# Kernel tuning notes

Hardware: AMD Instinct MI355X
Metric: run time of the kernel (lower is better)

The kernel has to match this reference:

```python
import math
import jax, jax.numpy as jnp
import numpy as np

S, B, H = 512, 64, 1024

def setup_inputs() -> dict:
    key = jax.random.key(0)
    ks = jax.random.split(key, 7)
    hidden = jax.random.normal(ks[0], (1, B, H), dtype=jnp.float32)
    encoder_outputs = jax.random.normal(ks[1], (S, B, H), dtype=jnp.float32)
    pe = jax.random.normal(ks[2], (B, S), dtype=jnp.float32)
    seq_mask = jax.random.bernoulli(ks[3], 0.1, (B, S))
    # nn.Linear(2H, H): weight (H, 2H), bias (H); nn.Linear(H, 1, bias=False): weight (1, H)
    Wa = jax.random.normal(ks[4], (H, 2 * H), dtype=jnp.float32) * (1.0 / math.sqrt(2 * H))
    ba = jax.random.normal(ks[5], (H,), dtype=jnp.float32) * 0.01
    Ws = jax.random.normal(ks[6], (1, H), dtype=jnp.float32) * (1.0 / math.sqrt(H))
    return {"hidden": hidden, "encoder_outputs": encoder_outputs, "pe": pe,
            "seq_mask": seq_mask, "Wa": Wa, "ba": ba, "Ws": Ws}

def reference(hidden, encoder_outputs, pe, seq_mask, Wa, ba, Ws):
    max_len, bsz, hdim = encoder_outputs.shape
    factor = 1.0 / math.sqrt(hdim)
    scale = factor * math.log(max_len)
    # repeat hidden along seq dim, concat on feature dim -> (S, B, 2H)
    h_rep = jnp.broadcast_to(hidden, (max_len, bsz, hdim))
    energy_in = jnp.concatenate([h_rep, encoder_outputs], axis=2)  # (S, B, 2H)
    e = jax.nn.relu(jnp.einsum('sbf,hf->sbh', energy_in, Wa) + ba)  # (S, B, H)
    attn = scale * jnp.einsum('sbh,oh->sbo', e, Ws)[..., 0]          # (S, B)
    attn = attn.T + pe                                               # (B, S)
    attn = jnp.where(seq_mask, jnp.float32(-1e12), attn)
    attn = jax.nn.softmax(attn, axis=1)
    return attn[:, None, :]  # (B, 1, S)
```

## Files before the change

### kernel.cpp

```cpp
#include <hip/hip_runtime.h>
#include <hip/hip_bf16.h>

#define S_LEN 512
#define HDIM 1024
#define H2 2048

typedef float f32x4 __attribute__((ext_vector_type(4)));
typedef float f32x2 __attribute__((ext_vector_type(2)));
typedef __bf16 bf16x8 __attribute__((ext_vector_type(8)));

#define E1_PITCH 258
__global__ __launch_bounds__(256) void k_e1(const float* __restrict__ hidden,
                                            const float* __restrict__ Wa,
                                            const float* __restrict__ ba,
                                            float* __restrict__ e1) {
    __shared__ float hsh[64 * E1_PITCH];
    int h = blockIdx.x * 4 + (threadIdx.x >> 6);
    int lane = threadIdx.x & 63;
    const float* wrow = Wa + (size_t)h * H2;
    float acc = 0.f;
    for (int k0 = 0; k0 < HDIM; k0 += 256) {
        __syncthreads();
        for (int idx = threadIdx.x; idx < 4096; idx += 256) {
            int b = idx >> 6, ck = (idx & 63) << 2;
            f32x4 v = *(const f32x4*)(hidden + b * HDIM + k0 + ck);
            f32x2 lo; lo[0] = v[0]; lo[1] = v[1];
            f32x2 hi; hi[0] = v[2]; hi[1] = v[3];
            *(f32x2*)(hsh + b * E1_PITCH + ck) = lo;
            *(f32x2*)(hsh + b * E1_PITCH + ck + 2) = hi;
        }
        __syncthreads();
        const float* wr = wrow + k0;
        const float* hb = hsh + lane * E1_PITCH;
#pragma unroll 8
        for (int kk = 0; kk < 256; kk += 4) {
            f32x4 w = *(const f32x4*)(wr + kk);
            f32x2 h01 = *(const f32x2*)(hb + kk);
            f32x2 h23 = *(const f32x2*)(hb + kk + 2);
            acc += w[0] * h01[0] + w[1] * h01[1] + w[2] * h23[0] + w[3] * h23[1];
        }
    }
    e1[lane * HDIM + h] = acc + ba[h];
}

__global__ __launch_bounds__(256) void k_packB(const float* __restrict__ Wa,
                                               unsigned short* __restrict__ wsB,
                                               float* __restrict__ logits) {
    int ci = blockIdx.x * 256 + threadIdx.x;
    if (ci < S_LEN * 64) logits[ci] = 0.f;
    int tile = ci >> 9;
    int wi = ci & 511;
    int row = wi >> 2;
    int slot = wi & 3;
    int nt = tile >> 5, kt = tile & 31;
    int n = nt * 128 + row;
    int kk = kt * 32 + ((slot ^ ((row >> 1) & 3)) << 3);
    const float* src = Wa + (size_t)n * H2 + HDIM + kk;
    f32x4 a = *(const f32x4*)src;
    f32x4 b = *(const f32x4*)(src + 4);
    bf16x8 o;
    o[0] = (__bf16)a[0]; o[1] = (__bf16)a[1]; o[2] = (__bf16)a[2]; o[3] = (__bf16)a[3];
    o[4] = (__bf16)b[0]; o[5] = (__bf16)b[1]; o[6] = (__bf16)b[2]; o[7] = (__bf16)b[3];
    *(bf16x8*)(wsB + (size_t)ci * 8) = o;
}

__global__ __launch_bounds__(256, 3) void k_main(const float* __restrict__ enc,
                                                 const unsigned short* __restrict__ wsB,
                                                 const float* __restrict__ e1,
                                                 const float* __restrict__ Ws,
                                                 float* __restrict__ logits) {
    __shared__ __align__(16) char lds[49152];

    int i = blockIdx.x;
    int mt = ((i >> 6) << 3) | (i & 7);
    int nt = (i >> 3) & 7;
    int r0 = mt * 128;
    int n0 = nt * 128;

    int tid = threadIdx.x;
    int lane = tid & 63, wid = tid >> 6;
    int wr = wid >> 1, wc = wid & 1;
    int c = lane & 15, g = lane >> 4;

    int arow = tid >> 3;
    int aslot = tid & 7;
    int acol = (aslot ^ (arow & 7)) << 2;
    const float* asrc0 = enc + (size_t)(r0 + arow) * HDIM + acol;

    const unsigned short* bbase = wsB + ((size_t)(nt * 32) << 12);

    f32x4 acc[4][4] = {};

#define STAGE_AB(AOFF, BOFF, KT)                                                        \
    {                                                                                   \
        const float* as_ = asrc0 + (KT) * 32;                                           \
        _Pragma("unroll")                                                               \
        for (int it = 0; it < 4; ++it) {                                                \
            __builtin_amdgcn_global_load_lds(                                           \
                (const __attribute__((address_space(1))) void*)(as_ + (size_t)it * 32 * HDIM), \
                (__attribute__((address_space(3))) void*)(lds + (AOFF) + it * 4096 + wid * 1024), \
                16, 0, 0);                                                              \
        }                                                                               \
        const unsigned short* bs_ = bbase + ((size_t)(KT) << 12);                       \
        _Pragma("unroll")                                                               \
        for (int it = 0; it < 2; ++it) {                                                \
            __builtin_amdgcn_global_load_lds(                                           \
                (const __attribute__((address_space(1))) void*)(bs_ + (size_t)(tid + it * 256) * 8), \
                (__attribute__((address_space(3))) void*)(lds + (BOFF) + it * 4096 + wid * 1024), \
                16, 0, 0);                                                              \
        }                                                                               \
    }

    STAGE_AB(0, 32768, 0);

#pragma unroll 2
    for (int t = 0; t < 32; ++t) {
        int ca = (t & 1) ? 16384 : 0;
        int na = ca ^ 16384;
        int cbb = (t & 1) ? 40960 : 32768;
        int nb = cbb ^ 8192;
        int tn = (t < 31) ? t + 1 : 31;

        STAGE_AB(na, nb, tn);
        __builtin_amdgcn_sched_barrier(0);
        asm volatile("s_waitcnt vmcnt(6)" ::: "memory");
        __builtin_amdgcn_sched_barrier(0);
        __builtin_amdgcn_s_barrier();
        __builtin_amdgcn_sched_barrier(0);

        bf16x8 af[4], bfr[4];
#pragma unroll
        for (int m = 0; m < 4; ++m) {
            int rowa = wr * 64 + m * 16 + c;
            const char* pa = lds + ca + rowa * 128;
            int s0 = (2 * g) ^ (rowa & 7);
            f32x4 fa = *(const f32x4*)(pa + s0 * 16);
            f32x4 fb = *(const f32x4*)(pa + (s0 ^ 1) * 16);
            bf16x8 o;
            o[0] = (__bf16)fa[0]; o[1] = (__bf16)fa[1]; o[2] = (__bf16)fa[2]; o[3] = (__bf16)fa[3];
            o[4] = (__bf16)fb[0]; o[5] = (__bf16)fb[1]; o[6] = (__bf16)fb[2]; o[7] = (__bf16)fb[3];
            af[m] = o;
        }
#pragma unroll
        for (int n = 0; n < 4; ++n) {
            int rowb = wc * 64 + n * 16 + c;
            int sl = g ^ ((rowb >> 1) & 3);
            bfr[n] = *(const bf16x8*)(lds + cbb + rowb * 64 + sl * 16);
        }
        __builtin_amdgcn_s_setprio(1);
#pragma unroll
        for (int m = 0; m < 4; ++m)
#pragma unroll
            for (int n = 0; n < 4; ++n)
                acc[m][n] = __builtin_amdgcn_mfma_f32_16x16x32_bf16(af[m], bfr[n], acc[m][n], 0, 0, 0);
        __builtin_amdgcn_s_setprio(0);

        __builtin_amdgcn_sched_barrier(0);
        __builtin_amdgcn_s_barrier();
        __builtin_amdgcn_sched_barrier(0);
    }
    asm volatile("s_waitcnt vmcnt(0)" ::: "memory");

    float wsv[4];
#pragma unroll
    for (int n = 0; n < 4; ++n) wsv[n] = Ws[n0 + wc * 64 + n * 16 + c];

#pragma unroll
    for (int m = 0; m < 4; ++m) {
#pragma unroll
        for (int j = 0; j < 4; ++j) {
            int rl = wr * 64 + m * 16 + g * 4 + j;
            int r = r0 + rl;
            int b = r & 63, sidx = r >> 6;
            const float* e1b = e1 + b * HDIM + n0 + wc * 64;
            float pp = 0.f;
#pragma unroll
            for (int n = 0; n < 4; ++n) {
                float v = acc[m][n][j] + e1b[n * 16 + c];
                v = fmaxf(v, 0.f);
                pp += v * wsv[n];
            }
            pp += __shfl_xor(pp, 1);
            pp += __shfl_xor(pp, 2);
            pp += __shfl_xor(pp, 4);
            pp += __shfl_xor(pp, 8);
            if (c == 0) atomicAdd(&logits[b * S_LEN + sidx], pp);
        }
    }
#undef STAGE_AB
}

__global__ __launch_bounds__(512) void k_softmax(float* __restrict__ out,
                                                 const float* __restrict__ pe,
                                                 const int* __restrict__ mask,
                                                 float scale) {
    __shared__ float red[8];
    int b = blockIdx.x, s = threadIdx.x;
    int idx = (b << 9) + s;
    float acc = out[idx];
    float logit = (mask[idx] != 0) ? -1e12f : (scale * acc + pe[idx]);
    float m = logit;
#pragma unroll
    for (int o = 32; o >= 1; o >>= 1) m = fmaxf(m, __shfl_xor(m, o));
    if ((s & 63) == 0) red[s >> 6] = m;
    __syncthreads();
    float m2 = red[0];
#pragma unroll
    for (int i2 = 1; i2 < 8; ++i2) m2 = fmaxf(m2, red[i2]);
    float e = expf(logit - m2);
    float t = e;
#pragma unroll
    for (int o = 32; o >= 1; o >>= 1) t += __shfl_xor(t, o);
    __syncthreads();
    if ((s & 63) == 0) red[s >> 6] = t;
    __syncthreads();
    float tot = 0.f;
#pragma unroll
    for (int i2 = 0; i2 < 8; ++i2) tot += red[i2];
    out[idx] = e / tot;
}

extern "C" void kernel_launch(void* const* d_in, const int* in_sizes, int n_in,
                              void* d_out, int out_size, void* d_ws, size_t ws_size,
                              hipStream_t stream) {
    const float* hidden = (const float*)d_in[0];
    const float* enc    = (const float*)d_in[1];
    const float* pe     = (const float*)d_in[2];
    const int*   mask   = (const int*)d_in[3];
    const float* Wa     = (const float*)d_in[4];
    const float* ba     = (const float*)d_in[5];
    const float* Ws     = (const float*)d_in[6];
    float* out = (float*)d_out;

    float* e1 = (float*)d_ws;
    unsigned short* wsB = (unsigned short*)((char*)d_ws + 262144);

    const float scale = 0.19494764453248462f;

    k_e1<<<256, 256, 0, stream>>>(hidden, Wa, ba, e1);
    k_packB<<<512, 256, 0, stream>>>(Wa, wsB, out);
    k_main<<<2048, 256, 0, stream>>>(enc, wsB, e1, Ws, out);
    k_softmax<<<64, 512, 0, stream>>>(out, pe, mask, scale);
}
```

Before: 355.7 us.

## Pre-pack encoder outputs to swizzled bf16 and triple-buffer the GEMM pipeline

Adds a k_packA kernel that converts encoder_outputs from fp32 to bf16 once per call, writing them in the same swizzled tile layout already used for the weights. The main GEMM then loads bf16 tiles for both operands straight into LDS, with no per-tile fp32-to-bf16 conversion and half the A bytes staged per k-step. The loop moves from double to triple buffering, waits with vmcnt(4), and raises the occupancy hint to 4. The cost is an extra full pass over the large encoder tensor (fp32 read plus bf16 write), and another kernel launch.

Measured after the change: 400.1 us. 12.5% more time.

```diff
diff --git a/kernel.cpp b/kernel.cpp
--- a/kernel.cpp
+++ b/kernel.cpp
@@ -64,12 +64,31 @@
     *(bf16x8*)(wsB + (size_t)ci * 8) = o;
 }
 
-__global__ __launch_bounds__(256, 3) void k_main(const float* __restrict__ enc,
+__global__ __launch_bounds__(256) void k_packA(const float* __restrict__ enc,
+                                               unsigned short* __restrict__ wsA) {
+    int ci = blockIdx.x * 256 + threadIdx.x;
+    const float* src = enc + (size_t)ci * 8;
+    f32x4 a = *(const f32x4*)src;
+    f32x4 b = *(const f32x4*)(src + 4);
+    int row_g = ci >> 7;
+    int cchunk = ci & 127;
+    int kt = cchunk >> 2, slot_src = cchunk & 3;
+    int mt = row_g >> 7, row = row_g & 127;
+    int slot = slot_src ^ ((row >> 1) & 3);
+    size_t dst = ((((size_t)(mt * 32 + kt)) << 9) + (row << 2) + slot) << 3;
+    bf16x8 o;
+    o[0] = (__bf16)a[0]; o[1] = (__bf16)a[1]; o[2] = (__bf16)a[2]; o[3] = (__bf16)a[3];
+    o[4] = (__bf16)b[0]; o[5] = (__bf16)b[1]; o[6] = (__bf16)b[2]; o[7] = (__bf16)b[3];
+    *(bf16x8*)(wsA + dst) = o;
+}
+
+__global__ __launch_bounds__(256, 4) void k_main(const unsigned short* __restrict__ wsA,
                                                  const unsigned short* __restrict__ wsB,
                                                  const float* __restrict__ e1,
                                                  const float* __restrict__ Ws,
                                                  float* __restrict__ logits) {
-    __shared__ __align__(16) char lds[49152];
+    __shared__ __align__(16) unsigned short As[3][4096];
+    __shared__ __align__(16) unsigned short Bs[3][4096];
 
     int i = blockIdx.x;
     int mt = ((i >> 6) << 3) | (i & 7);
@@ -82,70 +101,57 @@
     int wr = wid >> 1, wc = wid & 1;
     int c = lane & 15, g = lane >> 4;
 
-    int arow = tid >> 3;
-    int aslot = tid & 7;
-    int acol = (aslot ^ (arow & 7)) << 2;
-    const float* asrc0 = enc + (size_t)(r0 + arow) * HDIM + acol;
-
+    const unsigned short* abase = wsA + ((size_t)(mt * 32) << 12);
     const unsigned short* bbase = wsB + ((size_t)(nt * 32) << 12);
 
     f32x4 acc[4][4] = {};
 
-#define STAGE_AB(AOFF, BOFF, KT)                                                        \
-    {                                                                                   \
-        const float* as_ = asrc0 + (KT) * 32;                                           \
-        _Pragma("unroll")                                                               \
-        for (int it = 0; it < 4; ++it) {                                                \
-            __builtin_amdgcn_global_load_lds(                                           \
-                (const __attribute__((address_space(1))) void*)(as_ + (size_t)it * 32 * HDIM), \
-                (__attribute__((address_space(3))) void*)(lds + (AOFF) + it * 4096 + wid * 1024), \
-                16, 0, 0);                                                              \
-        }                                                                               \
-        const unsigned short* bs_ = bbase + ((size_t)(KT) << 12);                       \
-        _Pragma("unroll")                                                               \
-        for (int it = 0; it < 2; ++it) {                                                \
-            __builtin_amdgcn_global_load_lds(                                           \
-                (const __attribute__((address_space(1))) void*)(bs_ + (size_t)(tid + it * 256) * 8), \
-                (__attribute__((address_space(3))) void*)(lds + (BOFF) + it * 4096 + wid * 1024), \
-                16, 0, 0);                                                              \
-        }                                                                               \
-    }
-
-    STAGE_AB(0, 32768, 0);
-
-#pragma unroll 2
-    for (int t = 0; t < 32; ++t) {
-        int ca = (t & 1) ? 16384 : 0;
-        int na = ca ^ 16384;
-        int cbb = (t & 1) ? 40960 : 32768;
-        int nb = cbb ^ 8192;
-        int tn = (t < 31) ? t + 1 : 31;
-
-        STAGE_AB(na, nb, tn);
-        __builtin_amdgcn_sched_barrier(0);
-        asm volatile("s_waitcnt vmcnt(6)" ::: "memory");
-        __builtin_amdgcn_sched_barrier(0);
-        __builtin_amdgcn_s_barrier();
+#define STAGE(BUF, KT)                                                                   \
+    {                                                                                    \
+        const unsigned short* as_ = abase + ((size_t)(KT) << 12);                        \
+        const unsigned short* bs_ = bbase + ((size_t)(KT) << 12);                        \
+        __builtin_amdgcn_global_load_lds(                                                \
+            (const __attribute__((address_space(1))) void*)(as_ + (size_t)tid * 8),      \
+            (__attribute__((address_space(3))) void*)((char*)As[BUF] + wid * 1024), 16, 0, 0); \
+        __builtin_amdgcn_global_load_lds(                                                \
+            (const __attribute__((address_space(1))) void*)(as_ + (size_t)(tid + 256) * 8), \
+            (__attribute__((address_space(3))) void*)((char*)As[BUF] + 4096 + wid * 1024), 16, 0, 0); \
+        __builtin_amdgcn_global_load_lds(                                                \
+            (const __attribute__((address_space(1))) void*)(bs_ + (size_t)tid * 8),      \
+            (__attribute__((address_space(3))) void*)((char*)Bs[BUF] + wid * 1024), 16, 0, 0); \
+        __builtin_amdgcn_global_load_lds(                                                \
+            (const __attribute__((address_space(1))) void*)(bs_ + (size_t)(tid + 256) * 8), \
+            (__attribute__((address_space(3))) void*)((char*)Bs[BUF] + 4096 + wid * 1024), 16, 0, 0); \
+    }
+
+    STAGE(0, 0);
+    STAGE(1, 1);
+    __builtin_amdgcn_sched_barrier(0);
+    asm volatile("s_waitcnt vmcnt(4)" ::: "memory");
+    __builtin_amdgcn_sched_barrier(0);
+    __builtin_amdgcn_s_barrier();
+    __builtin_amdgcn_sched_barrier(0);
+
+    for (int kt = 0; kt < 32; ++kt) {
+        int cur = kt % 3;
+        int nxt = (kt + 2) % 3;
+        int ks = (kt + 2 < 32) ? kt + 2 : 31;
+
+        STAGE(nxt, ks);
         __builtin_amdgcn_sched_barrier(0);
 
         bf16x8 af[4], bfr[4];
 #pragma unroll
         for (int m = 0; m < 4; ++m) {
-            int rowa = wr * 64 + m * 16 + c;
-            const char* pa = lds + ca + rowa * 128;
-            int s0 = (2 * g) ^ (rowa & 7);
-            f32x4 fa = *(const f32x4*)(pa + s0 * 16);
-            f32x4 fb = *(const f32x4*)(pa + (s0 ^ 1) * 16);
-            bf16x8 o;
-            o[0] = (__bf16)fa[0]; o[1] = (__bf16)fa[1]; o[2] = (__bf16)fa[2]; o[3] = (__bf16)fa[3];
-            o[4] = (__bf16)fb[0]; o[5] = (__bf16)fb[1]; o[6] = (__bf16)fb[2]; o[7] = (__bf16)fb[3];
-            af[m] = o;
+            int row = wr * 64 + m * 16 + c;
+            int slot = g ^ ((row >> 1) & 3);
+            af[m] = *(const bf16x8*)((const char*)As[cur] + row * 64 + slot * 16);
         }
 #pragma unroll
         for (int n = 0; n < 4; ++n) {
             int rowb = wc * 64 + n * 16 + c;
-            int sl = g ^ ((rowb >> 1) & 3);
-            bfr[n] = *(const bf16x8*)(lds + cbb + rowb * 64 + sl * 16);
+            int slot = g ^ ((rowb >> 1) & 3);
+            bfr[n] = *(const bf16x8*)((const char*)Bs[cur] + rowb * 64 + slot * 16);
         }
         __builtin_amdgcn_s_setprio(1);
 #pragma unroll
@@ -154,12 +160,15 @@
             for (int n = 0; n < 4; ++n)
                 acc[m][n] = __builtin_amdgcn_mfma_f32_16x16x32_bf16(af[m], bfr[n], acc[m][n], 0, 0, 0);
         __builtin_amdgcn_s_setprio(0);
-
+        __builtin_amdgcn_sched_barrier(0);
+
+        asm volatile("s_waitcnt vmcnt(4)" ::: "memory");
         __builtin_amdgcn_sched_barrier(0);
         __builtin_amdgcn_s_barrier();
         __builtin_amdgcn_sched_barrier(0);
     }
     asm volatile("s_waitcnt vmcnt(0)" ::: "memory");
+#undef STAGE
 
     float wsv[4];
 #pragma unroll
@@ -187,7 +196,6 @@
             if (c == 0) atomicAdd(&logits[b * S_LEN + sidx], pp);
         }
     }
-#undef STAGE_AB
 }
 
 __global__ __launch_bounds__(512) void k_softmax(float* __restrict__ out,
@@ -234,11 +242,13 @@
 
     float* e1 = (float*)d_ws;
     unsigned short* wsB = (unsigned short*)((char*)d_ws + 262144);
+    unsigned short* wsA = (unsigned short*)((char*)d_ws + 262144 + 2097152);
 
     const float scale = 0.19494764453248462f;
 
     k_e1<<<256, 256, 0, stream>>>(hidden, Wa, ba, e1);
     k_packB<<<512, 256, 0, stream>>>(Wa, wsB, out);
-    k_main<<<2048, 256, 0, stream>>>(enc, wsB, e1, Ws, out);
+    k_packA<<<16384, 256, 0, stream>>>(enc, wsA);
+    k_main<<<2048, 256, 0, stream>>>(wsA, wsB, e1, Ws, out);
     k_softmax<<<64, 512, 0, stream>>>(out, pe, mask, scale);
 }
```
